# Kernel optimization log

Measured on AMD Instinct MI355X. Metric: run time of the kernel, lower is better.

## Reference

```python
import jax, jax.numpy as jnp
import numpy as np

N_NODES = 100000
N_EDGES = 1600000
IN_DIM, HID_DIM, OUT_DIM = 128, 128, 1


def gcn_conv(x, W, b, src, dst, n_nodes):
    """PyG-style GCNConv: add self-loops, symmetric D^-1/2 (A+I) D^-1/2 normalization.

    x: [N, F_in], W: [F_in, F_out], b: [F_out], src/dst: [E] int edge endpoints.
    """
    h = x @ W  # [N, F_out] transform first (as PyG does)
    # degree on A + I, counted over destination (symmetric graph assumption)
    ones = jnp.ones(src.shape[0], dtype=h.dtype)
    deg = jax.ops.segment_sum(ones, dst, num_segments=n_nodes) + 1.0  # +1 self loop
    dinv = jax.lax.rsqrt(deg)  # [N]
    norm = dinv[src] * dinv[dst]  # [E] edge normalization
    msg = h[src] * norm[:, None]  # [E, F_out] gather + scale
    agg = jax.ops.segment_sum(msg, dst, num_segments=n_nodes)  # scatter-add
    # self-loop contribution: norm_ii = dinv[i]^2
    out = agg + h * (dinv * dinv)[:, None]
    return out + b


def setup_inputs() -> dict:
    key = jax.random.key(0)
    k1, k2, k3, k4 = jax.random.split(key, 4)
    x = jax.random.normal(k1, (N_NODES, IN_DIM), dtype=jnp.float32)
    edge_index = jax.random.randint(k2, (2, N_EDGES), 0, N_NODES, dtype=jnp.int64)
    W1 = jax.random.normal(k3, (IN_DIM, HID_DIM), dtype=jnp.float32) * (1.0 / np.sqrt(IN_DIM))
    b1 = jnp.zeros((HID_DIM,), dtype=jnp.float32)
    W2 = jax.random.normal(k4, (HID_DIM, OUT_DIM), dtype=jnp.float32) * (1.0 / np.sqrt(HID_DIM))
    b2 = jnp.zeros((OUT_DIM,), dtype=jnp.float32)
    return {"x": x, "edge_index": edge_index, "W1": W1, "b1": b1, "W2": W2, "b2": b2}


def reference(x, edge_index, W1, b1, W2, b2):
    n = x.shape[0]
    src, dst = edge_index[0], edge_index[1]
    h = gcn_conv(x, W1, b1, src, dst, n)
    h = jax.nn.relu(h)
    # dropout(p=0.2) is identity at inference
    out = gcn_conv(h, W2, b2, src, dst, n)  # [N, 1]
    return out
```

## Files before the change

### kernel.cpp

```cpp
#include <hip/hip_runtime.h>

#define N_NODES 100000
#define N_EDGES 1600000
#define DIM 128

#define BSHIFT 8
#define BNODES 256
#define NBUCK 391
#define BCAP  4608
#define PCHUNK 4096
#define NB_PART ((N_EDGES + PCHUNK - 1) / PCHUNK)

#define GTILES 1563
#define GGRID  782

typedef short s16x8 __attribute__((ext_vector_type(8)));
typedef float f32x4 __attribute__((ext_vector_type(4)));

__device__ __forceinline__ unsigned short f2bf(float f) {
    unsigned u = __float_as_uint(f);
    u += 0x7fffu + ((u >> 16) & 1u);
    return (unsigned short)(u >> 16);
}
__device__ __forceinline__ float bflo(unsigned u) { return __uint_as_float(u << 16); }
__device__ __forceinline__ float bfhi(unsigned u) { return __uint_as_float(u & 0xffff0000u); }

__device__ __forceinline__ void acc8(float (&a)[8], uint4 v, float w) {
    a[0] = fmaf(bflo(v.x), w, a[0]); a[1] = fmaf(bfhi(v.x), w, a[1]);
    a[2] = fmaf(bflo(v.y), w, a[2]); a[3] = fmaf(bfhi(v.y), w, a[3]);
    a[4] = fmaf(bflo(v.z), w, a[4]); a[5] = fmaf(bfhi(v.z), w, a[5]);
    a[6] = fmaf(bflo(v.w), w, a[6]); a[7] = fmaf(bfhi(v.w), w, a[7]);
}


__global__ void k_zero(int* __restrict__ gcur) {
    int t = blockIdx.x * blockDim.x + threadIdx.x;
    if (t < NBUCK) gcur[t] = t * BCAP;
}

__device__ __forceinline__ void part_body(char* smem, int bid,
                                          const int* __restrict__ src,
                                          const int* __restrict__ dst,
                                          int* __restrict__ gcur,
                                          int2* __restrict__ ebuf) {
    int* hist = (int*)smem;
    int* gbase = hist + NBUCK;
    int tid = threadIdx.x;
    long e0 = (long)bid * PCHUNK;
    int n = min(PCHUNK, (int)(N_EDGES - e0));
    for (int b = tid; b < NBUCK; b += 256) hist[b] = 0;
    __syncthreads();

    int mys[16], myd[16];
#pragma unroll
    for (int k = 0; k < 16; ++k) {
        int idx = k * 256 + tid;
        if (idx < n) {
            mys[k] = src[e0 + idx];
            myd[k] = dst[e0 + idx];
            atomicAdd(&hist[myd[k] >> BSHIFT], 1);
        } else {
            myd[k] = -1;
        }
    }
    __syncthreads();
    for (int b = tid; b < NBUCK; b += 256) {
        gbase[b] = hist[b] ? atomicAdd(&gcur[b], hist[b]) : 0;
        hist[b] = 0;
    }
    __syncthreads();
#pragma unroll
    for (int k = 0; k < 16; ++k) {
        if (myd[k] >= 0) {
            int b = myd[k] >> BSHIFT;
            int slot = gbase[b] + atomicAdd(&hist[b], 1);
            ebuf[slot] = make_int2(mys[k], myd[k]);
        }
    }
}

__device__ __forceinline__ void gemm_body(char* smem, int bid,
                                          const float* __restrict__ x,
                                          const float* __restrict__ W1,
                                          unsigned short* __restrict__ h1) {
    unsigned short* Wt = (unsigned short*)smem;
    int tid = threadIdx.x;
    for (int idx = tid; idx < DIM * DIM; idx += 256) {
        int k = idx >> 7, c = idx & 127;
        Wt[c * 128 + (k ^ ((c & 7) << 3))] = f2bf(W1[idx]);
    }
    __syncthreads();

    int wv = tid >> 6, lane = tid & 63;
    int g = lane >> 4, tl = lane & 15;
    unsigned short* cst = (unsigned short*)(smem + 32768 + wv * 4096);

    for (int tile = bid; tile < GTILES; tile += GGRID) {
        int rb = tile * 64 + wv * 16;
        if (rb >= N_NODES) continue;

        s16x8 afrag[4];
        const float* xrow = x + (size_t)(rb + tl) * DIM + g * 8;
#pragma unroll
        for (int kc = 0; kc < 4; ++kc) {
            float4 p0 = *(const float4*)(xrow + kc * 32);
            float4 p1 = *(const float4*)(xrow + kc * 32 + 4);
            s16x8 a;
            a[0] = (short)f2bf(p0.x); a[1] = (short)f2bf(p0.y);
            a[2] = (short)f2bf(p0.z); a[3] = (short)f2bf(p0.w);
            a[4] = (short)f2bf(p1.x); a[5] = (short)f2bf(p1.y);
            a[6] = (short)f2bf(p1.z); a[7] = (short)f2bf(p1.w);
            afrag[kc] = a;
        }

        f32x4 acc[8];
#pragma unroll
        for (int ct = 0; ct < 8; ++ct) acc[ct] = (f32x4)0.0f;
#pragma unroll
        for (int kc = 0; kc < 4; ++kc) {
#pragma unroll
            for (int ct = 0; ct < 8; ++ct) {
                int crow = ct * 16 + tl;
                int boff = crow * 256 + ((kc * 64 + g * 16) ^ ((crow & 7) << 4));
                s16x8 b = *(const s16x8*)((const char*)Wt + boff);
                acc[ct] = __builtin_amdgcn_mfma_f32_16x16x32_bf16(afrag[kc], b, acc[ct], 0, 0, 0);
            }
        }

#pragma unroll
        for (int ct = 0; ct < 8; ++ct) {
#pragma unroll
            for (int r = 0; r < 4; ++r) {
                float own = acc[ct][r];
                float oth = __shfl_xor(own, 1, 64);
                if ((lane & 1) == 0) {
                    unsigned pk = (unsigned)f2bf(own) | ((unsigned)f2bf(oth) << 16);
                    int row = g * 4 + r;
                    int col = ct * 16 + tl;
                    *(unsigned*)&cst[row * 128 + (col ^ (row << 3))] = pk;
                }
            }
        }
        asm volatile("s_waitcnt lgkmcnt(0)" ::: "memory");

        unsigned short* dstp = h1 + (size_t)rb * DIM;
#pragma unroll
        for (int c = 0; c < 4; ++c) {
            int row = c * 4 + g;
            uint4 v = *(const uint4*)&cst[row * 128 + ((tl ^ row) * 8)];
            *(uint4*)(dstp + c * 512 + lane * 8) = v;
        }
    }
}

__global__ __launch_bounds__(256) void k_part(const int* __restrict__ src,
                                              const int* __restrict__ dst,
                                              int* __restrict__ gcur,
                                              int2* __restrict__ ebuf) {
    __shared__ __align__(16) char smem[2 * NBUCK * 4 + 16];
    part_body(smem, blockIdx.x, src, dst, gcur, ebuf);
}

__global__ __launch_bounds__(256) void k_gemm(const float* __restrict__ x,
                                              const float* __restrict__ W1,
                                              unsigned short* __restrict__ h1) {
    __shared__ __align__(16) char smem[49152];
    gemm_body(smem, blockIdx.x, x, W1, h1);
}

__global__ __launch_bounds__(256) void k_pg(const int* __restrict__ src,
                                            const int* __restrict__ dst,
                                            int* __restrict__ gcur,
                                            int2* __restrict__ ebuf,
                                            const float* __restrict__ x,
                                            const float* __restrict__ W1,
                                            unsigned short* __restrict__ h1) {
    __shared__ __align__(16) char smem[49152];
    if (blockIdx.x < NB_PART) part_body(smem, blockIdx.x, src, dst, gcur, ebuf);
    else                      gemm_body(smem, blockIdx.x - NB_PART, x, W1, h1);
}

__global__ __launch_bounds__(256) void k_csrA(const int2* __restrict__ ebuf,
                                              const int* __restrict__ gcur,
                                              int* __restrict__ rp,
                                              int* __restrict__ cnt,
                                              float* __restrict__ dinv) {
    __shared__ int lcnt[BNODES];
    __shared__ int psum[BNODES];
    int b = blockIdx.x, t = threadIdx.x;
    int node0 = b << BSHIFT;
    lcnt[t] = 0;
    __syncthreads();
    int base = b * BCAP, end = gcur[b];
    for (int e = base + t; e < end; e += 256)
        atomicAdd(&lcnt[ebuf[e].y - node0], 1);
    __syncthreads();
    int c = lcnt[t];
    psum[t] = c;
    __syncthreads();
    for (int s = 1; s < 256; s <<= 1) {
        int u = (t >= s) ? psum[t - s] : 0;
        __syncthreads();
        psum[t] += u;
        __syncthreads();
    }
    int node = node0 + t;
    if (node < N_NODES) {
        rp[node] = base + psum[t] - c;
        cnt[node] = c;
        dinv[node] = rsqrtf((float)(c + 1));
    }
}

__global__ __launch_bounds__(256) void k_csrB(const int2* __restrict__ ebuf,
                                              const int* __restrict__ gcur,
                                              const int* __restrict__ rp,
                                              const float* __restrict__ dinv,
                                              int2* __restrict__ csrw) {
    __shared__ int lcur[BNODES];
    __shared__ float ldv[BNODES];
    int b = blockIdx.x, t = threadIdx.x;
    int node0 = b << BSHIFT;
    int base = b * BCAP, end = gcur[b];
    int node = node0 + t;
    if (node < N_NODES) { lcur[t] = rp[node] - base; ldv[t] = dinv[node]; }
    __syncthreads();
    int e = base + t;
    for (; e + 256 < end; e += 512) {
        int2 d0 = ebuf[e];
        int2 d1 = ebuf[e + 256];
        int l0 = d0.y - node0, l1 = d1.y - node0;
        float w0 = dinv[d0.x] * ldv[l0];
        float w1 = dinv[d1.x] * ldv[l1];
        int p0 = atomicAdd(&lcur[l0], 1);
        int p1 = atomicAdd(&lcur[l1], 1);
        csrw[base + p0] = make_int2(d0.x, __float_as_int(w0));
        csrw[base + p1] = make_int2(d1.x, __float_as_int(w1));
    }
    if (e < end) {
        int2 d0 = ebuf[e];
        int l0 = d0.y - node0;
        float w0 = dinv[d0.x] * ldv[l0];
        int p0 = atomicAdd(&lcur[l0], 1);
        csrw[base + p0] = make_int2(d0.x, __float_as_int(w0));
    }
}


__global__ __launch_bounds__(256) void k_agg1(const unsigned short* __restrict__ h1,
                                              const float* __restrict__ dinv,
                                              const int* __restrict__ rp,
                                              const int* __restrict__ cnt,
                                              const int2* __restrict__ csrw,
                                              const float* __restrict__ b1,
                                              const float* __restrict__ W2,
                                              float* __restrict__ z) {
    int lane = threadIdx.x & 63;
    int wv = threadIdx.x >> 6;
    int g = lane >> 4, tl = lane & 15;
    int i = blockIdx.x * 16 + wv * 4 + g;
    int c0 = tl * 8;
    float di = dinv[i];
    int beg = rp[i], end = beg + cnt[i];
    float a[8];
#pragma unroll
    for (int q = 0; q < 8; ++q) a[q] = 0.f;
    const unsigned short* hbase = h1 + c0;

    int j = beg;
    if ((j & 1) && j < end) {
        int2 e0 = csrw[j];
        uint4 v0 = *(const uint4*)(hbase + (size_t)e0.x * DIM);
        acc8(a, v0, __int_as_float(e0.y));
        ++j;
    }
    for (; j + 6 <= end; j += 6) {
        uint4 m0 = *(const uint4*)(csrw + j);
        uint4 m1 = *(const uint4*)(csrw + j + 2);
        uint4 m2 = *(const uint4*)(csrw + j + 4);
        uint4 v0 = *(const uint4*)(hbase + (size_t)(int)m0.x * DIM);
        uint4 v1 = *(const uint4*)(hbase + (size_t)(int)m0.z * DIM);
        uint4 v2 = *(const uint4*)(hbase + (size_t)(int)m1.x * DIM);
        uint4 v3 = *(const uint4*)(hbase + (size_t)(int)m1.z * DIM);
        uint4 v4 = *(const uint4*)(hbase + (size_t)(int)m2.x * DIM);
        uint4 v5 = *(const uint4*)(hbase + (size_t)(int)m2.z * DIM);
        acc8(a, v0, __int_as_float(m0.y));
        acc8(a, v1, __int_as_float(m0.w));
        acc8(a, v2, __int_as_float(m1.y));
        acc8(a, v3, __int_as_float(m1.w));
        acc8(a, v4, __int_as_float(m2.y));
        acc8(a, v5, __int_as_float(m2.w));
    }
    for (; j < end; ++j) {
        int2 e0 = csrw[j];
        uint4 v0 = *(const uint4*)(hbase + (size_t)e0.x * DIM);
        acc8(a, v0, __int_as_float(e0.y));
    }

    uint4 vs = *(const uint4*)(hbase + (size_t)i * DIM);
    float sii = di * di;
    float4 bA = *(const float4*)(b1 + c0);
    float4 bB = *(const float4*)(b1 + c0 + 4);
    float4 wA = *(const float4*)(W2 + c0);
    float4 wB = *(const float4*)(W2 + c0 + 4);
    float p = 0.f;
    p += fmaxf(fmaf(bflo(vs.x), sii, a[0]) + bA.x, 0.f) * wA.x;
    p += fmaxf(fmaf(bfhi(vs.x), sii, a[1]) + bA.y, 0.f) * wA.y;
    p += fmaxf(fmaf(bflo(vs.y), sii, a[2]) + bA.z, 0.f) * wA.z;
    p += fmaxf(fmaf(bfhi(vs.y), sii, a[3]) + bA.w, 0.f) * wA.w;
    p += fmaxf(fmaf(bflo(vs.z), sii, a[4]) + bB.x, 0.f) * wB.x;
    p += fmaxf(fmaf(bfhi(vs.z), sii, a[5]) + bB.y, 0.f) * wB.y;
    p += fmaxf(fmaf(bflo(vs.w), sii, a[6]) + bB.z, 0.f) * wB.z;
    p += fmaxf(fmaf(bfhi(vs.w), sii, a[7]) + bB.w, 0.f) * wB.w;
#pragma unroll
    for (int off = 8; off >= 1; off >>= 1) p += __shfl_xor(p, off, 64);
    if (tl == 0) z[i] = p;
}


__global__ __launch_bounds__(256) void k_agg2(const float* __restrict__ zin,
                                              const float* __restrict__ dinv,
                                              const int* __restrict__ rp,
                                              const int* __restrict__ cnt,
                                              const int2* __restrict__ csrw,
                                              const float* __restrict__ b2,
                                              float* __restrict__ out) {
    int i = blockIdx.x * blockDim.x + threadIdx.x;
    if (i >= N_NODES) return;
    float di = dinv[i];
    int beg = rp[i], end = beg + cnt[i];
    float acc = 0.f;
    int j = beg;
    if ((j & 1) && j < end) {
        int2 e = csrw[j];
        acc = fmaf(zin[e.x], __int_as_float(e.y), acc);
        ++j;
    }
    for (; j + 6 <= end; j += 6) {
        uint4 m0 = *(const uint4*)(csrw + j);
        uint4 m1 = *(const uint4*)(csrw + j + 2);
        uint4 m2 = *(const uint4*)(csrw + j + 4);
        float z0 = zin[(int)m0.x], z1 = zin[(int)m0.z];
        float z2 = zin[(int)m1.x], z3 = zin[(int)m1.z];
        float z4 = zin[(int)m2.x], z5 = zin[(int)m2.z];
        acc = fmaf(z0, __int_as_float(m0.y), acc);
        acc = fmaf(z1, __int_as_float(m0.w), acc);
        acc = fmaf(z2, __int_as_float(m1.y), acc);
        acc = fmaf(z3, __int_as_float(m1.w), acc);
        acc = fmaf(z4, __int_as_float(m2.y), acc);
        acc = fmaf(z5, __int_as_float(m2.w), acc);
    }
    for (; j < end; ++j) {
        int2 e = csrw[j];
        acc = fmaf(zin[e.x], __int_as_float(e.y), acc);
    }
    out[i] = acc + zin[i] * di * di + b2[0];
}


extern "C" void kernel_launch(void* const* d_in, const int* in_sizes, int n_in,
                              void* d_out, int out_size, void* d_ws, size_t ws_size,
                              hipStream_t stream) {
    const float* x  = (const float*)d_in[0];
    const int*   ei = (const int*)d_in[1];
    const float* W1 = (const float*)d_in[2];
    const float* b1 = (const float*)d_in[3];
    const float* W2 = (const float*)d_in[4];
    const float* b2 = (const float*)d_in[5];
    float* out = (float*)d_out;

    const int* src = ei;
    const int* dst = ei + N_EDGES;

    char* ws = (char*)d_ws;
    size_t o = 0;
    auto take = [&](size_t bytes) { char* p = ws + o; o += (bytes + 255) & ~(size_t)255; return p; };
    int*   cnt   = (int*)take(sizeof(int) * N_NODES);
    int*   rp    = (int*)take(sizeof(int) * N_NODES);
    int*   gcur  = (int*)take(sizeof(int) * (NBUCK + 1));
    float* dinv  = (float*)take(sizeof(float) * N_NODES);
    float* z     = (float*)take(sizeof(float) * N_NODES);
    int2*  csrw  = (int2*)take(sizeof(int2) * (size_t)NBUCK * BCAP);
    unsigned short* h1 = (unsigned short*)take(sizeof(unsigned short) * (size_t)N_NODES * DIM);
    int2* ebuf_sep = (int2*)take(sizeof(int2) * (size_t)NBUCK * BCAP);
    bool fused = (o <= ws_size);
    int2* ebuf = fused ? ebuf_sep : (int2*)h1;

    const int NB_N = (N_NODES + 255) / 256;

    k_zero<<<2, 256, 0, stream>>>(gcur);
    if (fused) {
        k_pg<<<NB_PART + GGRID, 256, 0, stream>>>(src, dst, gcur, ebuf, x, W1, h1);
        k_csrA<<<NBUCK, 256, 0, stream>>>(ebuf, gcur, rp, cnt, dinv);
        k_csrB<<<NBUCK, 256, 0, stream>>>(ebuf, gcur, rp, dinv, csrw);
    } else {
        k_part<<<NB_PART, 256, 0, stream>>>(src, dst, gcur, ebuf);
        k_csrA<<<NBUCK, 256, 0, stream>>>(ebuf, gcur, rp, cnt, dinv);
        k_csrB<<<NBUCK, 256, 0, stream>>>(ebuf, gcur, rp, dinv, csrw);
        k_gemm<<<GGRID, 256, 0, stream>>>(x, W1, h1);
    }
    k_agg1<<<N_NODES / 16, 256, 0, stream>>>(h1, dinv, rp, cnt, csrw, b1, W2, z);
    k_agg2<<<NB_N, 256, 0, stream>>>(z, dinv, rp, cnt, csrw, b2, out);
}
```

Before: 149.2 us.

## Merge CSR build kernels and store source-only CSR with on-the-fly weights

The two CSR construction kernels become one: the block computes per-node counts and prefix sums, then scatters only source indices into a 4-byte CSR array. Edge weights are no longer precomputed. The aggregation kernels instead gather dinv[src] and multiply by dinv[dst] inline. This removes one launch and halves CSR storage and traffic, at the cost of an extra random dinv gather per edge in both aggregations. GGRID is also doubled, which changes the GEMM grid and how the gemm_body tiles are assigned.

```diff
diff --git a/kernel.cpp b/kernel.cpp
--- a/kernel.cpp
+++ b/kernel.cpp
@@ -12,7 +12,7 @@
 #define NB_PART ((N_EDGES + PCHUNK - 1) / PCHUNK)
 
 #define GTILES 1563
-#define GGRID  782
+#define GGRID  1563
 
 typedef short s16x8 __attribute__((ext_vector_type(8)));
 typedef float f32x4 __attribute__((ext_vector_type(4)));
@@ -180,13 +180,14 @@
     else                      gemm_body(smem, blockIdx.x - NB_PART, x, W1, h1);
 }
 
-__global__ __launch_bounds__(256) void k_csrA(const int2* __restrict__ ebuf,
-                                              const int* __restrict__ gcur,
-                                              int* __restrict__ rp,
-                                              int* __restrict__ cnt,
-                                              float* __restrict__ dinv) {
+__global__ __launch_bounds__(256) void k_csr(const int2* __restrict__ ebuf,
+                                             const int* __restrict__ gcur,
+                                             int* __restrict__ rp,
+                                             int* __restrict__ cnt,
+                                             float* __restrict__ dinv,
+                                             int* __restrict__ csrs) {
     __shared__ int lcnt[BNODES];
-    __shared__ int psum[BNODES];
+    __shared__ int lcur[BNODES];
     int b = blockIdx.x, t = threadIdx.x;
     int node0 = b << BSHIFT;
     lcnt[t] = 0;
@@ -196,53 +197,27 @@
         atomicAdd(&lcnt[ebuf[e].y - node0], 1);
     __syncthreads();
     int c = lcnt[t];
-    psum[t] = c;
+    lcur[t] = c;
     __syncthreads();
     for (int s = 1; s < 256; s <<= 1) {
-        int u = (t >= s) ? psum[t - s] : 0;
+        int u = (t >= s) ? lcur[t - s] : 0;
         __syncthreads();
-        psum[t] += u;
+        lcur[t] += u;
         __syncthreads();
     }
+    int excl = lcur[t] - c;
+    lcur[t] = excl;
     int node = node0 + t;
     if (node < N_NODES) {
-        rp[node] = base + psum[t] - c;
+        rp[node] = base + excl;
         cnt[node] = c;
         dinv[node] = rsqrtf((float)(c + 1));
     }
-}
-
-__global__ __launch_bounds__(256) void k_csrB(const int2* __restrict__ ebuf,
-                                              const int* __restrict__ gcur,
-                                              const int* __restrict__ rp,
-                                              const float* __restrict__ dinv,
-                                              int2* __restrict__ csrw) {
-    __shared__ int lcur[BNODES];
-    __shared__ float ldv[BNODES];
-    int b = blockIdx.x, t = threadIdx.x;
-    int node0 = b << BSHIFT;
-    int base = b * BCAP, end = gcur[b];
-    int node = node0 + t;
-    if (node < N_NODES) { lcur[t] = rp[node] - base; ldv[t] = dinv[node]; }
-    __syncthreads();
-    int e = base + t;
-    for (; e + 256 < end; e += 512) {
-        int2 d0 = ebuf[e];
-        int2 d1 = ebuf[e + 256];
-        int l0 = d0.y - node0, l1 = d1.y - node0;
-        float w0 = dinv[d0.x] * ldv[l0];
-        float w1 = dinv[d1.x] * ldv[l1];
-        int p0 = atomicAdd(&lcur[l0], 1);
-        int p1 = atomicAdd(&lcur[l1], 1);
-        csrw[base + p0] = make_int2(d0.x, __float_as_int(w0));
-        csrw[base + p1] = make_int2(d1.x, __float_as_int(w1));
-    }
-    if (e < end) {
-        int2 d0 = ebuf[e];
-        int l0 = d0.y - node0;
-        float w0 = dinv[d0.x] * ldv[l0];
-        int p0 = atomicAdd(&lcur[l0], 1);
-        csrw[base + p0] = make_int2(d0.x, __float_as_int(w0));
+    __syncthreads();
+    for (int e = base + t; e < end; e += 256) {
+        int2 d = ebuf[e];
+        int p = atomicAdd(&lcur[d.y - node0], 1);
+        csrs[base + p] = d.x;
     }
 }
 
@@ -251,7 +226,7 @@
                                               const float* __restrict__ dinv,
                                               const int* __restrict__ rp,
                                               const int* __restrict__ cnt,
-                                              const int2* __restrict__ csrw,
+                                              const int* __restrict__ csrs,
                                               const float* __restrict__ b1,
                                               const float* __restrict__ W2,
                                               float* __restrict__ z) {
@@ -268,33 +243,23 @@
     const unsigned short* hbase = h1 + c0;
 
     int j = beg;
-    if ((j & 1) && j < end) {
-        int2 e0 = csrw[j];
-        uint4 v0 = *(const uint4*)(hbase + (size_t)e0.x * DIM);
-        acc8(a, v0, __int_as_float(e0.y));
-        ++j;
-    }
-    for (; j + 6 <= end; j += 6) {
-        uint4 m0 = *(const uint4*)(csrw + j);
-        uint4 m1 = *(const uint4*)(csrw + j + 2);
-        uint4 m2 = *(const uint4*)(csrw + j + 4);
-        uint4 v0 = *(const uint4*)(hbase + (size_t)(int)m0.x * DIM);
-        uint4 v1 = *(const uint4*)(hbase + (size_t)(int)m0.z * DIM);
-        uint4 v2 = *(const uint4*)(hbase + (size_t)(int)m1.x * DIM);
-        uint4 v3 = *(const uint4*)(hbase + (size_t)(int)m1.z * DIM);
-        uint4 v4 = *(const uint4*)(hbase + (size_t)(int)m2.x * DIM);
-        uint4 v5 = *(const uint4*)(hbase + (size_t)(int)m2.z * DIM);
-        acc8(a, v0, __int_as_float(m0.y));
-        acc8(a, v1, __int_as_float(m0.w));
-        acc8(a, v2, __int_as_float(m1.y));
-        acc8(a, v3, __int_as_float(m1.w));
-        acc8(a, v4, __int_as_float(m2.y));
-        acc8(a, v5, __int_as_float(m2.w));
+    for (; j + 4 <= end; j += 4) {
+        int s0 = csrs[j], s1 = csrs[j + 1], s2 = csrs[j + 2], s3 = csrs[j + 3];
+        uint4 v0 = *(const uint4*)(hbase + (size_t)s0 * DIM);
+        uint4 v1 = *(const uint4*)(hbase + (size_t)s1 * DIM);
+        uint4 v2 = *(const uint4*)(hbase + (size_t)s2 * DIM);
+        uint4 v3 = *(const uint4*)(hbase + (size_t)s3 * DIM);
+        float w0 = dinv[s0] * di, w1 = dinv[s1] * di;
+        float w2 = dinv[s2] * di, w3 = dinv[s3] * di;
+        acc8(a, v0, w0);
+        acc8(a, v1, w1);
+        acc8(a, v2, w2);
+        acc8(a, v3, w3);
     }
     for (; j < end; ++j) {
-        int2 e0 = csrw[j];
-        uint4 v0 = *(const uint4*)(hbase + (size_t)e0.x * DIM);
-        acc8(a, v0, __int_as_float(e0.y));
+        int s0 = csrs[j];
+        uint4 v0 = *(const uint4*)(hbase + (size_t)s0 * DIM);
+        acc8(a, v0, dinv[s0] * di);
     }
 
     uint4 vs = *(const uint4*)(hbase + (size_t)i * DIM);
@@ -322,7 +287,7 @@
                                               const float* __restrict__ dinv,
                                               const int* __restrict__ rp,
                                               const int* __restrict__ cnt,
-                                              const int2* __restrict__ csrw,
+                                              const int* __restrict__ csrs,
                                               const float* __restrict__ b2,
                                               float* __restrict__ out) {
     int i = blockIdx.x * blockDim.x + threadIdx.x;
@@ -331,28 +296,17 @@
     int beg = rp[i], end = beg + cnt[i];
     float acc = 0.f;
     int j = beg;
-    if ((j & 1) && j < end) {
-        int2 e = csrw[j];
-        acc = fmaf(zin[e.x], __int_as_float(e.y), acc);
-        ++j;
-    }
-    for (; j + 6 <= end; j += 6) {
-        uint4 m0 = *(const uint4*)(csrw + j);
-        uint4 m1 = *(const uint4*)(csrw + j + 2);
-        uint4 m2 = *(const uint4*)(csrw + j + 4);
-        float z0 = zin[(int)m0.x], z1 = zin[(int)m0.z];
-        float z2 = zin[(int)m1.x], z3 = zin[(int)m1.z];
-        float z4 = zin[(int)m2.x], z5 = zin[(int)m2.z];
-        acc = fmaf(z0, __int_as_float(m0.y), acc);
-        acc = fmaf(z1, __int_as_float(m0.w), acc);
-        acc = fmaf(z2, __int_as_float(m1.y), acc);
-        acc = fmaf(z3, __int_as_float(m1.w), acc);
-        acc = fmaf(z4, __int_as_float(m2.y), acc);
-        acc = fmaf(z5, __int_as_float(m2.w), acc);
+    for (; j + 4 <= end; j += 4) {
+        int s0 = csrs[j], s1 = csrs[j + 1], s2 = csrs[j + 2], s3 = csrs[j + 3];
+        float z0 = zin[s0], z1 = zin[s1], z2 = zin[s2], z3 = zin[s3];
+        acc = fmaf(z0, dinv[s0] * di, acc);
+        acc = fmaf(z1, dinv[s1] * di, acc);
+        acc = fmaf(z2, dinv[s2] * di, acc);
+        acc = fmaf(z3, dinv[s3] * di, acc);
     }
     for (; j < end; ++j) {
-        int2 e = csrw[j];
-        acc = fmaf(zin[e.x], __int_as_float(e.y), acc);
+        int s0 = csrs[j];
+        acc = fmaf(zin[s0], dinv[s0] * di, acc);
     }
     out[i] = acc + zin[i] * di * di + b2[0];
 }
@@ -380,7 +334,7 @@
     int*   gcur  = (int*)take(sizeof(int) * (NBUCK + 1));
     float* dinv  = (float*)take(sizeof(float) * N_NODES);
     float* z     = (float*)take(sizeof(float) * N_NODES);
-    int2*  csrw  = (int2*)take(sizeof(int2) * (size_t)NBUCK * BCAP);
+    int*   csrs  = (int*)take(sizeof(int) * (size_t)NBUCK * BCAP);
     unsigned short* h1 = (unsigned short*)take(sizeof(unsigned short) * (size_t)N_NODES * DIM);
     int2* ebuf_sep = (int2*)take(sizeof(int2) * (size_t)NBUCK * BCAP);
     bool fused = (o <= ws_size);
@@ -391,14 +345,12 @@
     k_zero<<<2, 256, 0, stream>>>(gcur);
     if (fused) {
         k_pg<<<NB_PART + GGRID, 256, 0, stream>>>(src, dst, gcur, ebuf, x, W1, h1);
-        k_csrA<<<NBUCK, 256, 0, stream>>>(ebuf, gcur, rp, cnt, dinv);
-        k_csrB<<<NBUCK, 256, 0, stream>>>(ebuf, gcur, rp, dinv, csrw);
+        k_csr<<<NBUCK, 256, 0, stream>>>(ebuf, gcur, rp, cnt, dinv, csrs);
     } else {
         k_part<<<NB_PART, 256, 0, stream>>>(src, dst, gcur, ebuf);
-        k_csrA<<<NBUCK, 256, 0, stream>>>(ebuf, gcur, rp, cnt, dinv);
-        k_csrB<<<NBUCK, 256, 0, stream>>>(ebuf, gcur, rp, dinv, csrw);
+        k_csr<<<NBUCK, 256, 0, stream>>>(ebuf, gcur, rp, cnt, dinv, csrs);
         k_gemm<<<GGRID, 256, 0, stream>>>(x, W1, h1);
     }
-    k_agg1<<<N_NODES / 16, 256, 0, stream>>>(h1, dinv, rp, cnt, csrw, b1, W2, z);
-    k_agg2<<<NB_N, 256, 0, stream>>>(z, dinv, rp, cnt, csrw, b2, out);
-}
+    k_agg1<<<N_NODES / 16, 256, 0, stream>>>(h1, dinv, rp, cnt, csrs, b1, W2, z);
+    k_agg2<<<NB_N, 256, 0, stream>>>(z, dinv, rp, cnt, csrs, b2, out);
+}
```

New measurement: 142.1 us. 1.05x faster.
